# Kernel optimization log

Hardware: AMD Instinct MI355X
Metric: run time of the kernel (lower is better)

## Reference

```python
import jax, jax.numpy as jnp
import numpy as np
from jax import lax

B, N, C = 4, 1024, 384
H, G, K = 6, 2, 10
GD = C // G   # group dim = 192
HD = C // H   # head dim = 64
SCALE = HD ** -0.5
LN_EPS = 1e-5


def _sqdist(a, b):
    # a: [..., M, 3], b: [..., N, 3] -> squared euclid dist [..., M, N]
    return (jnp.sum(a * a, -1)[..., :, None]
            - 2.0 * jnp.einsum('...mc,...nc->...mn', a, b)
            + jnp.sum(b * b, -1)[..., None, :])


def _layernorm(x, g, b):
    mu = jnp.mean(x, -1, keepdims=True)
    var = jnp.mean(jnp.square(x - mu), -1, keepdims=True)
    return (x - mu) * lax.rsqrt(var + LN_EPS) * g + b


def _forward(q, q_pos, Wq, Wk, Wv, Wvoff, W1, b1, ln_g, ln_b, W2, Wproj, bproj):
    # self-attention path: v = q, v_pos = q_pos
    bidx = jnp.arange(B)[:, None, None]
    # KNN over positions: idx [B, N, K]
    d = _sqdist(q_pos, q_pos)
    _, idx = lax.top_k(-d, K)
    qp = q @ Wq                       # [B, N, C]
    v_off = q @ Wvoff                 # [B, N, C]
    local_v = v_off[bidx, idx]        # [B, N, K, C]
    # split channels into groups: 'b n k (g c) -> b g n k c'
    off_local_v = local_v.reshape(B, N, K, G, GD).transpose(0, 3, 1, 2, 4)
    group_q = qp.reshape(B, N, G, GD).transpose(0, 2, 1, 3)      # [B, G, N, GD]
    shift_feat = jnp.concatenate(
        [off_local_v, jnp.broadcast_to(group_q[:, :, :, None, :], (B, G, N, K, GD))], -1)
    h = _layernorm(shift_feat @ W1 + b1, ln_g, ln_b)
    h = jax.nn.gelu(h, approximate=False)
    offset = jnp.tanh(h @ W2)                                    # [B, G, N, K, 3]
    local_v_pos = q_pos[bidx, idx]                               # [B, N, K, 3]
    shift_pos = (local_v_pos[:, None] + offset).reshape(B, G, N * K, 3)
    # three_nn: 3 nearest v_pos points for each shifted point (squared dists, as in CUDA kernel)
    v_pos_g = jnp.broadcast_to(q_pos[:, None], (B, G, N, 3))
    d2 = _sqdist(shift_pos, v_pos_g)                             # [B, G, N*K, N]
    neg_d3, idx3 = lax.top_k(-d2, 3)
    dist3 = -neg_d3                                              # ascending
    rec = 1.0 / (dist3 + 1e-8)
    w = rec / jnp.sum(rec, -1, keepdims=True)                    # [B, G, N*K, 3]
    # three_interpolate on grouped v features
    v_g = q.reshape(B, N, G, GD).transpose(0, 2, 1, 3)           # [B, G, N, GD]
    gathered = v_g[jnp.arange(B)[:, None, None, None],
                   jnp.arange(G)[None, :, None, None], idx3]      # [B, G, N*K, 3, GD]
    interp = jnp.sum(w[..., None] * gathered, 3)                 # [B, G, N*K, GD]
    # '(b g) (n k) c -> b n k (g c)'
    interp = interp.reshape(B, G, N, K, GD).transpose(0, 2, 3, 1, 4).reshape(B, N, K, C)
    # local cross attention: 1 query vs K keys per token per head
    kk = (interp @ Wk).reshape(B, N, K, H, HD)
    vv = (interp @ Wv).reshape(B, N, K, H, HD)
    qh = qp.reshape(B, N, H, HD)
    attn = jnp.einsum('bnhd,bnkhd->bnhk', qh, kk) * SCALE
    attn = jax.nn.softmax(attn, -1)
    out = jnp.einsum('bnhk,bnkhd->bnhd', attn, vv).reshape(B, N, C)
    return out @ Wproj + bproj


def setup_inputs() -> dict:
    key = jax.random.key(0)
    ks = jax.random.split(key, 12)
    s = 0.02
    return {
        'q': jax.random.normal(ks[0], (B, N, C), jnp.float32),
        'q_pos': jax.random.normal(ks[1], (B, N, 3), jnp.float32),
        'Wq': s * jax.random.normal(ks[2], (C, C), jnp.float32),
        'Wk': s * jax.random.normal(ks[3], (C, C), jnp.float32),
        'Wv': s * jax.random.normal(ks[4], (C, C), jnp.float32),
        'Wvoff': s * jax.random.normal(ks[5], (C, C), jnp.float32),
        'W1': s * jax.random.normal(ks[6], (2 * GD, C), jnp.float32),
        'b1': jnp.zeros((C,), jnp.float32),
        'ln_g': jnp.ones((C,), jnp.float32),
        'ln_b': jnp.zeros((C,), jnp.float32),
        'W2': s * jax.random.normal(ks[7], (C, 3), jnp.float32),
        'Wproj': s * jax.random.normal(ks[8], (C, C), jnp.float32),
        'bproj': jnp.zeros((C,), jnp.float32),
    }


def reference(q, q_pos, Wq, Wk, Wv, Wvoff, W1, b1, ln_g, ln_b, W2, Wproj, bproj):
    return _forward(q, q_pos, Wq, Wk, Wv, Wvoff, W1, b1, ln_g, ln_b, W2, Wproj, bproj)
```

## Files before the change

kernel.cpp:

```cpp
#include <hip/hip_runtime.h>
#include <math.h>

constexpr int B_ = 4;
constexpr int N_ = 1024;
constexpr int C_ = 384;
constexpr int G_ = 2;
constexpr int K_ = 10;
constexpr int GD_ = 192;
constexpr int NK_ = N_ * K_;
constexpr int M2_ = B_ * G_ * N_ * K_;
constexpr float SCALE_ = 0.125f;
constexpr float MARGIN_ = 4e-4f;

__device__ __forceinline__ bool lless(double da, int ia, double db, int ib) {
  return (da < db) || (da == db && ia < ib);
}
__device__ __forceinline__ void lmin2(double& rd, int& ri, double ad, int ai,
                                      double bd, int bi) {
  bool t = lless(bd, bi, ad, ai);
  rd = t ? bd : ad; ri = t ? bi : ai;
}
__device__ __forceinline__ void lmax2(double& rd, int& ri, double ad, int ai,
                                      double bd, int bi) {
  bool t = lless(ad, ai, bd, bi);
  rd = t ? bd : ad; ri = t ? bi : ai;
}
__device__ __forceinline__ bool llessf(float da, int ia, float db, int ib) {
  return (da < db) || (da == db && ia < ib);
}
__device__ __forceinline__ void lmin2f(float& rd, int& ri, float ad, int ai,
                                       float bd, int bi) {
  bool t = llessf(bd, bi, ad, ai);
  rd = t ? bd : ad; ri = t ? bi : ai;
}
__device__ __forceinline__ void lmax2f(float& rd, int& ri, float ad, int ai,
                                       float bd, int bi) {
  bool t = llessf(ad, ai, bd, bi);
  rd = t ? bd : ad; ri = t ? bi : ai;
}

__global__ void k_zero(int* __restrict__ cnt) { cnt[0] = 0; }

__global__ void k_sqnorm2(const float* __restrict__ q_pos, double* __restrict__ s64,
                          float* __restrict__ s32) {
  int i = blockIdx.x * blockDim.x + threadIdx.x;
  if (i >= B_ * N_) return;
  double x = q_pos[3 * i], y = q_pos[3 * i + 1], z = q_pos[3 * i + 2];
  double v = x * x + y * y + z * z;
  s64[i] = v;
  s32[i] = (float)v;
}

__global__ __launch_bounds__(256) void k_knn10_w(const float* __restrict__ q_pos,
                                                 const double* __restrict__ s,
                                                 int* __restrict__ idx10) {
  int wid = (blockIdx.x * blockDim.x + threadIdx.x) >> 6;
  int lane = threadIdx.x & 63;
  if (wid >= B_ * N_) return;
  int b = wid / N_;
  double px = q_pos[3 * wid], py = q_pos[3 * wid + 1], pz = q_pos[3 * wid + 2];
  double sm = s[wid];
  const float* bp = q_pos + b * N_ * 3;
  const double* bs = s + b * N_;
  double d[K_]; int ix[K_];
  #pragma unroll
  for (int j = 0; j < K_; j++) { d[j] = INFINITY; ix[j] = 0x7fffffff; }
  for (int n0 = 0; n0 < N_; n0 += 64) {
    int n = n0 + lane;
    double dot = px * (double)bp[3 * n] + py * (double)bp[3 * n + 1] +
                 pz * (double)bp[3 * n + 2];
    double v = (sm - 2.0 * dot) + bs[n];
    bool c[K_];
    #pragma unroll
    for (int j = 0; j < K_; j++) c[j] = lless(v, n, d[j], ix[j]);
    #pragma unroll
    for (int j = K_ - 1; j >= 1; j--) {
      d[j]  = c[j] ? (c[j - 1] ? d[j - 1] : v) : d[j];
      ix[j] = c[j] ? (c[j - 1] ? ix[j - 1] : n) : ix[j];
    }
    d[0]  = c[0] ? v : d[0];
    ix[0] = c[0] ? n : ix[0];
  }
  #pragma unroll
  for (int off = 1; off < 64; off <<= 1) {
    double bd[K_]; int bi[K_];
    #pragma unroll
    for (int j = 0; j < K_; j++) {
      bd[j] = __shfl_xor(d[j], off);
      bi[j] = __shfl_xor(ix[j], off);
    }
    double md[K_]; int mi[K_];
    #pragma unroll
    for (int r = 0; r < K_; r++) {
      double m; int mj;
      lmin2(m, mj, d[r], ix[r], bd[r], bi[r]);
      #pragma unroll
      for (int j = 1; j <= r; j++) {
        double t; int ti;
        lmax2(t, ti, d[j - 1], ix[j - 1], bd[r - j], bi[r - j]);
        lmin2(m, mj, m, mj, t, ti);
      }
      md[r] = m; mi[r] = mj;
    }
    #pragma unroll
    for (int j = 0; j < K_; j++) { d[j] = md[j]; ix[j] = mi[j]; }
  }
  if (lane == 0) {
    #pragma unroll
    for (int j = 0; j < K_; j++) idx10[wid * K_ + j] = ix[j];
  }
}

template <int TM>
__global__ __launch_bounds__(384) void k_gemmSA(const float* __restrict__ A,
                                                const float* __restrict__ W,
                                                const float* __restrict__ bias,
                                                float* __restrict__ out, int M) {
  int c = threadIdx.x;
  int r0 = blockIdx.x * TM;
  float acc[TM];
  #pragma unroll
  for (int r = 0; r < TM; r++) acc[r] = 0.f;
  #pragma unroll 4
  for (int j = 0; j < C_; j++) {
    float w = W[j * C_ + c];
    #pragma unroll
    for (int r = 0; r < TM; r++) acc[r] = fmaf(A[(r0 + r) * C_ + j], w, acc[r]);
  }
  float bv = bias ? bias[c] : 0.f;
  #pragma unroll
  for (int r = 0; r < TM; r++) out[(r0 + r) * C_ + c] = acc[r] + bv;
}

__global__ __launch_bounds__(384) void k_prepM(const float* __restrict__ Wvoff,
                                               const float* __restrict__ Wq,
                                               const float* __restrict__ W1,
                                               float* __restrict__ M1f,
                                               float* __restrict__ M2f) {
  int g = blockIdx.x / C_;
  int k = blockIdx.x % C_;
  int c = threadIdx.x;
  const float* wv = Wvoff + k * C_ + g * GD_;
  const float* wq = Wq + k * C_ + g * GD_;
  double a1 = 0.0, a2 = 0.0;
  for (int d = 0; d < GD_; d++) {
    a1 += (double)wv[d] * (double)W1[d * C_ + c];
    a2 += (double)wq[d] * (double)W1[(GD_ + d) * C_ + c];
  }
  M1f[(g * C_ + k) * C_ + c] = (float)a1;
  M2f[(g * C_ + k) * C_ + c] = (float)a2;
}

template <int TM>
__global__ __launch_bounds__(384) void k_Y32(const float* __restrict__ q,
                                             const float* __restrict__ M1f,
                                             const float* __restrict__ M2f,
                                             float* __restrict__ Y1f,
                                             float* __restrict__ Y2f) {
  int c = threadIdx.x;
  int g = blockIdx.y;
  int r0 = blockIdx.x * TM;
  float a1[TM], a2[TM];
  #pragma unroll
  for (int r = 0; r < TM; r++) { a1[r] = 0.f; a2[r] = 0.f; }
  const float* m1 = M1f + (size_t)(g * C_) * C_ + c;
  const float* m2 = M2f + (size_t)(g * C_) * C_ + c;
  for (int k = 0; k < C_; k++) {
    float v1 = m1[(size_t)k * C_];
    float v2 = m2[(size_t)k * C_];
    #pragma unroll
    for (int r = 0; r < TM; r++) {
      float av = q[(r0 + r) * C_ + k];
      a1[r] = fmaf(av, v1, a1[r]);
      a2[r] = fmaf(av, v2, a2[r]);
    }
  }
  #pragma unroll
  for (int r = 0; r < TM; r++) {
    Y1f[((size_t)(r0 + r) * G_ + g) * C_ + c] = a1[r];
    Y2f[((size_t)(r0 + r) * G_ + g) * C_ + c] = a2[r];
  }
}

__global__ __launch_bounds__(256) void k_mlp32(const float* __restrict__ Y1f,
                                               const float* __restrict__ Y2f,
                                               const int* __restrict__ idx10,
                                               const float* __restrict__ q_pos,
                                               const float* __restrict__ b1,
                                               const float* __restrict__ ln_g,
                                               const float* __restrict__ ln_b,
                                               const float* __restrict__ W2,
                                               float* __restrict__ shift32) {
  int w_ = threadIdx.x >> 6, l = threadIdx.x & 63;
  int row = blockIdx.x * 4 + w_;
  int k = row % K_; int t = row / K_;
  int n = t % N_; t /= N_;
  int g = t % G_; int b = t / G_;
  int j = idx10[(b * N_ + n) * K_ + k];
  const float* y1 = Y1f + ((size_t)(b * N_ + j) * G_ + g) * C_;
  const float* y2 = Y2f + ((size_t)(b * N_ + n) * G_ + g) * C_;
  float x[6];
  #pragma unroll
  for (int jj = 0; jj < 6; jj++) {
    int col = l + 64 * jj;
    x[jj] = y1[col] + y2[col] + b1[col];
  }
  float sum = ((((x[0] + x[1]) + x[2]) + x[3]) + x[4]) + x[5];
  #pragma unroll
  for (int off = 1; off < 64; off <<= 1) sum += __shfl_xor(sum, off);
  float mu = sum * (1.0f / 384.0f);
  float sq = 0.f;
  #pragma unroll
  for (int jj = 0; jj < 6; jj++) { float dd = x[jj] - mu; sq = fmaf(dd, dd, sq); }
  #pragma unroll
  for (int off = 1; off < 64; off <<= 1) sq += __shfl_xor(sq, off);
  float var = sq * (1.0f / 384.0f);
  float rstd = 1.0f / sqrtf(var + 1e-5f);
  float ge[6];
  #pragma unroll
  for (int jj = 0; jj < 6; jj++) {
    int col = l + 64 * jj;
    float nv = (x[jj] - mu) * rstd * ln_g[col] + ln_b[col];
    ge[jj] = 0.5f * nv * (1.0f + erff(nv * 0.70710678118654752f));
  }
  float o3[3];
  #pragma unroll
  for (int o = 0; o < 3; o++) {
    float p = 0.f;
    #pragma unroll
    for (int jj = 0; jj < 6; jj++) {
      int col = l + 64 * jj;
      p = fmaf(ge[jj], W2[col * 3 + o], p);
    }
    #pragma unroll
    for (int off = 1; off < 64; off <<= 1) p += __shfl_xor(p, off);
    o3[o] = tanhf(p);
  }
  if (l == 0) {
    int gi = b * N_ + j;
    shift32[(size_t)row * 3 + 0] = q_pos[gi * 3 + 0] + o3[0];
    shift32[(size_t)row * 3 + 1] = q_pos[gi * 3 + 1] + o3[1];
    shift32[(size_t)row * 3 + 2] = q_pos[gi * 3 + 2] + o3[2];
  }
}

__global__ __launch_bounds__(256) void k_top4(const float* __restrict__ shift32,
                                              const float* __restrict__ q_pos,
                                              const float* __restrict__ s32,
                                              const float* __restrict__ q,
                                              float* __restrict__ interp,
                                              int* __restrict__ flags,
                                              int* __restrict__ cnt) {
  int wid = (blockIdx.x * blockDim.x + threadIdx.x) >> 6;
  int lane = threadIdx.x & 63;
  int m = wid % NK_; int t = wid / NK_;
  int g = t % G_; int b = t / G_;
  float px = shift32[(size_t)wid * 3], py = shift32[(size_t)wid * 3 + 1],
        pz = shift32[(size_t)wid * 3 + 2];
  float sp = px * px + py * py + pz * pz;
  const float* bp = q_pos + b * N_ * 3;
  const float* bs = s32 + b * N_;
  float d[4]; int ix[4];
  #pragma unroll
  for (int j = 0; j < 4; j++) { d[j] = INFINITY; ix[j] = 0x7fffffff; }
  for (int n0 = 0; n0 < N_; n0 += 64) {
    int n = n0 + lane;
    float dot = px * bp[3 * n] + py * bp[3 * n + 1] + pz * bp[3 * n + 2];
    float v = (sp - 2.0f * dot) + bs[n];
    bool c[4];
    #pragma unroll
    for (int j = 0; j < 4; j++) c[j] = llessf(v, n, d[j], ix[j]);
    #pragma unroll
    for (int j = 3; j >= 1; j--) {
      d[j]  = c[j] ? (c[j - 1] ? d[j - 1] : v) : d[j];
      ix[j] = c[j] ? (c[j - 1] ? ix[j - 1] : n) : ix[j];
    }
    d[0]  = c[0] ? v : d[0];
    ix[0] = c[0] ? n : ix[0];
  }
  #pragma unroll
  for (int off = 1; off < 64; off <<= 1) {
    float bd[4]; int bi[4];
    #pragma unroll
    for (int j = 0; j < 4; j++) {
      bd[j] = __shfl_xor(d[j], off);
      bi[j] = __shfl_xor(ix[j], off);
    }
    float md[4]; int mi[4];
    #pragma unroll
    for (int r = 0; r < 4; r++) {
      float mm; int mj;
      lmin2f(mm, mj, d[r], ix[r], bd[r], bi[r]);
      #pragma unroll
      for (int j = 1; j <= r; j++) {
        float tt; int ti;
        lmax2f(tt, ti, d[j - 1], ix[j - 1], bd[r - j], bi[r - j]);
        lmin2f(mm, mj, mm, mj, tt, ti);
      }
      md[r] = mm; mi[r] = mj;
    }
    #pragma unroll
    for (int j = 0; j < 4; j++) { d[j] = md[j]; ix[j] = mi[j]; }
  }
  if (d[3] - d[2] < MARGIN_) {
    if (lane == 0) {
      int pos = atomicAdd(cnt, 1);
      flags[pos] = wid;
    }
    return;
  }
  float r0 = 1.0f / (d[0] + 1e-8f);
  float r1 = 1.0f / (d[1] + 1e-8f);
  float r2 = 1.0f / (d[2] + 1e-8f);
  float rs = (r0 + r1) + r2;
  float w0 = r0 / rs, w1 = r1 / rs, w2 = r2 / rs;
  const float* qb = q + (size_t)b * N_ * C_ + g * GD_;
  const float* p0 = qb + (size_t)ix[0] * C_;
  const float* p1 = qb + (size_t)ix[1] * C_;
  const float* p2 = qb + (size_t)ix[2] * C_;
  int n_ = m / K_, k_ = m % K_;
  float* op = interp + (((size_t)(b * N_ + n_) * K_ + k_) * C_) + g * GD_;
  #pragma unroll
  for (int cc0 = 0; cc0 < GD_; cc0 += 64) {
    int cc = cc0 + lane;
    op[cc] = (w0 * p0[cc] + w1 * p1[cc]) + w2 * p2[cc];
  }
}

__global__ __launch_bounds__(256) void k_fix(const int* __restrict__ cnt,
                                             const int* __restrict__ flags,
                                             const float* __restrict__ q,
                                             const float* __restrict__ Wvoff,
                                             const float* __restrict__ Wq,
                                             const float* __restrict__ W1,
                                             const int* __restrict__ idx10,
                                             const float* __restrict__ q_pos,
                                             const double* __restrict__ s64,
                                             const float* __restrict__ b1,
                                             const float* __restrict__ ln_g,
                                             const float* __restrict__ ln_b,
                                             const float* __restrict__ W2,
                                             float* __restrict__ interp) {
  __shared__ double vbuf[4][2][GD_];
  int w_ = threadIdx.x >> 6;
  int gwid = blockIdx.x * 4 + w_;
  int lane = threadIdx.x & 63;
  int nwaves = gridDim.x * 4;
  int total = cnt[0];
  for (int i = gwid; i < total; i += nwaves) {
    int wid = __builtin_amdgcn_readfirstlane(flags[i]);
    int m = wid % NK_; int t = wid / NK_;
    int g = t % G_; int b = t / G_;
    int n_ = m / K_, k_ = m % K_;
    int j = __builtin_amdgcn_readfirstlane(idx10[(b * N_ + n_) * K_ + k_]);
    const float* qj = q + (size_t)(b * N_ + j) * C_;
    const float* qn = q + (size_t)(b * N_ + n_) * C_;
    const float* wvo = Wvoff + g * GD_;
    const float* wqg = Wq + g * GD_;
    double a0 = 0.0, a1 = 0.0, a2 = 0.0, b0 = 0.0, b1a = 0.0, b2 = 0.0;
    for (int tt = 0; tt < C_; tt++) {
      double qjt = (double)qj[tt];
      double qnt = (double)qn[tt];
      const float* r1 = wvo + (size_t)tt * C_;
      const float* r2 = wqg + (size_t)tt * C_;
      a0 += qjt * (double)r1[lane];
      a1 += qjt * (double)r1[lane + 64];
      a2 += qjt * (double)r1[lane + 128];
      b0 += qnt * (double)r2[lane];
      b1a += qnt * (double)r2[lane + 64];
      b2 += qnt * (double)r2[lane + 128];
    }
    vbuf[w_][0][lane] = a0; vbuf[w_][0][lane + 64] = a1; vbuf[w_][0][lane + 128] = a2;
    vbuf[w_][1][lane] = b0; vbuf[w_][1][lane + 64] = b1a; vbuf[w_][1][lane + 128] = b2;
    double x[6];
    #pragma unroll
    for (int jj = 0; jj < 6; jj++) x[jj] = 0.0;
    for (int d = 0; d < GD_; d++) {
      double v1d = vbuf[w_][0][d];
      double v2d = vbuf[w_][1][d];
      const float* w1t = W1 + (size_t)d * C_;
      const float* w1b = W1 + (size_t)(GD_ + d) * C_;
      #pragma unroll
      for (int jj = 0; jj < 6; jj++) {
        int col = lane + 64 * jj;
        x[jj] += v1d * (double)w1t[col] + v2d * (double)w1b[col];
      }
    }
    #pragma unroll
    for (int jj = 0; jj < 6; jj++) x[jj] += (double)b1[lane + 64 * jj];
    double sum = ((((x[0] + x[1]) + x[2]) + x[3]) + x[4]) + x[5];
    #pragma unroll
    for (int off = 1; off < 64; off <<= 1) sum += __shfl_xor(sum, off);
    double mu = sum / 384.0;
    double sq = 0.0;
    #pragma unroll
    for (int jj = 0; jj < 6; jj++) { double dd = x[jj] - mu; sq += dd * dd; }
    #pragma unroll
    for (int off = 1; off < 64; off <<= 1) sq += __shfl_xor(sq, off);
    double var = sq / 384.0;
    double rstd = 1.0 / sqrt(var + 1e-5);
    double ge[6];
    #pragma unroll
    for (int jj = 0; jj < 6; jj++) {
      int col = lane + 64 * jj;
      double nv = (x[jj] - mu) * rstd * (double)ln_g[col] + (double)ln_b[col];
      ge[jj] = 0.5 * nv * (1.0 + erf(nv * 0.70710678118654752440));
    }
    double o3[3];
    #pragma unroll
    for (int o = 0; o < 3; o++) {
      double p = 0.0;
      #pragma unroll
      for (int jj = 0; jj < 6; jj++) {
        int col = lane + 64 * jj;
        p += ge[jj] * (double)W2[col * 3 + o];
      }
      #pragma unroll
      for (int off = 1; off < 64; off <<= 1) p += __shfl_xor(p, off);
      o3[o] = tanh(p);
    }
    int gi = b * N_ + j;
    double px = (double)q_pos[gi * 3 + 0] + o3[0];
    double py = (double)q_pos[gi * 3 + 1] + o3[1];
    double pz = (double)q_pos[gi * 3 + 2] + o3[2];
    double sp = px * px + py * py + pz * pz;
    const float* bp = q_pos + b * N_ * 3;
    const double* bs = s64 + b * N_;
    double d0 = INFINITY, d1 = INFINITY, d2 = INFINITY;
    int i0 = 0x7fffffff, i1 = 0x7fffffff, i2 = 0x7fffffff;
    for (int n = lane; n < N_; n += 64) {
      double dot = px * (double)bp[3 * n] + py * (double)bp[3 * n + 1] +
                   pz * (double)bp[3 * n + 2];
      double dd = (sp - 2.0 * dot) + bs[n];
      bool c0 = lless(dd, n, d0, i0);
      bool c1 = lless(dd, n, d1, i1);
      bool c2 = lless(dd, n, d2, i2);
      double nd2 = c2 ? (c1 ? d1 : dd) : d2; int ni2 = c2 ? (c1 ? i1 : n) : i2;
      double nd1 = c1 ? (c0 ? d0 : dd) : d1; int ni1 = c1 ? (c0 ? i0 : n) : i1;
      double nd0 = c0 ? dd : d0;             int ni0 = c0 ? n : i0;
      d0 = nd0; d1 = nd1; d2 = nd2; i0 = ni0; i1 = ni1; i2 = ni2;
    }
    #pragma unroll
    for (int off = 1; off < 64; off <<= 1) {
      double e0 = __shfl_xor(d0, off), e1 = __shfl_xor(d1, off), e2 = __shfl_xor(d2, off);
      int j0 = __shfl_xor(i0, off), j1 = __shfl_xor(i1, off), j2 = __shfl_xor(i2, off);
      double mnd, mxd, p1d, q1d, q2d, q3d, q4d, t1d, t2d;
      int mni, mxi, p1i, q1i, q2i, q3i, q4i, t1i, t2i;
      lmin2(mnd, mni, d0, i0, e0, j0);
      lmax2(mxd, mxi, d0, i0, e0, j0);
      lmin2(p1d, p1i, d1, i1, e1, j1);
      lmin2(t1d, t1i, p1d, p1i, mxd, mxi);
      lmax2(q1d, q1i, d1, i1, e0, j0);
      lmax2(q2d, q2i, d0, i0, e1, j1);
      lmin2(q3d, q3i, q1d, q1i, q2d, q2i);
      lmin2(q4d, q4i, d2, i2, e2, j2);
      lmin2(t2d, t2i, q3d, q3i, q4d, q4i);
      d0 = mnd; i0 = mni; d1 = t1d; i1 = t1i; d2 = t2d; i2 = t2i;
    }
    double r0 = 1.0 / (d0 + 1e-8);
    double r1 = 1.0 / (d1 + 1e-8);
    double r2 = 1.0 / (d2 + 1e-8);
    double rs = (r0 + r1) + r2;
    float w0 = (float)(r0 / rs), w1 = (float)(r1 / rs), w2 = (float)(r2 / rs);
    const float* qb = q + (size_t)b * N_ * C_ + g * GD_;
    const float* p0 = qb + (size_t)i0 * C_;
    const float* p1 = qb + (size_t)i1 * C_;
    const float* p2 = qb + (size_t)i2 * C_;
    float* op = interp + (((size_t)(b * N_ + n_) * K_ + k_) * C_) + g * GD_;
    #pragma unroll
    for (int cc0 = 0; cc0 < GD_; cc0 += 64) {
      int cc = cc0 + lane;
      op[cc] = (w0 * p0[cc] + w1 * p1[cc]) + w2 * p2[cc];
    }
  }
}

__global__ __launch_bounds__(256) void k_T(const float* __restrict__ Wk,
                                           float* __restrict__ WkT) {
  int i = blockIdx.x * blockDim.x + threadIdx.x;
  if (i >= C_ * C_) return;
  int r = i / C_, c = i % C_;
  WkT[c * C_ + r] = Wk[i];
}

template <int TM>
__global__ __launch_bounds__(384) void k_U(const float* __restrict__ qp,
                                           const float* __restrict__ WkT,
                                           float* __restrict__ U) {
  int c = threadIdx.x;
  int r0 = blockIdx.x * TM;
  for (int h = 0; h < 6; h++) {
    float acc[TM];
    #pragma unroll
    for (int r = 0; r < TM; r++) acc[r] = 0.f;
    #pragma unroll 4
    for (int dd = 0; dd < 64; dd++) {
      float w = WkT[(h * 64 + dd) * C_ + c];
      #pragma unroll
      for (int r = 0; r < TM; r++)
        acc[r] = fmaf(qp[(r0 + r) * C_ + h * 64 + dd], w, acc[r]);
    }
    #pragma unroll
    for (int r = 0; r < TM; r++) U[((size_t)(r0 + r) * 6 + h) * C_ + c] = acc[r];
  }
}

__global__ __launch_bounds__(256) void k_attn2(const float* __restrict__ interp,
                                               float* __restrict__ Umix) {
  int wid = blockIdx.x * 4 + (threadIdx.x >> 6);
  int lane = threadIdx.x & 63;
  int bn = wid / 6;
  float* urow = Umix + (size_t)wid * C_;
  float u[6];
  #pragma unroll
  for (int j = 0; j < 6; j++) u[j] = urow[lane + 64 * j];
  float logit[K_];
  #pragma unroll
  for (int k = 0; k < K_; k++) {
    const float* ip = interp + ((size_t)bn * K_ + k) * C_;
    float p = 0.f;
    #pragma unroll
    for (int j = 0; j < 6; j++) p = fmaf(ip[lane + 64 * j], u[j], p);
    #pragma unroll
    for (int off = 1; off < 64; off <<= 1) p += __shfl_xor(p, off);
    logit[k] = p * SCALE_;
  }
  float mx = logit[0];
  #pragma unroll
  for (int k = 1; k < K_; k++) mx = fmaxf(mx, logit[k]);
  float e[K_], se = 0.f;
  #pragma unroll
  for (int k = 0; k < K_; k++) { e[k] = expf(logit[k] - mx); se += e[k]; }
  float inv = 1.0f / se;
  #pragma unroll
  for (int k = 0; k < K_; k++) e[k] *= inv;
  #pragma unroll
  for (int j = 0; j < 6; j++) {
    float mv = 0.f;
    #pragma unroll
    for (int k = 0; k < K_; k++)
      mv = fmaf(e[k], interp[((size_t)bn * K_ + k) * C_ + lane + 64 * j], mv);
    urow[lane + 64 * j] = mv;
  }
}

template <int TM>
__global__ __launch_bounds__(384) void k_out(const float* __restrict__ mix,
                                             const float* __restrict__ Wv,
                                             float* __restrict__ attn_out) {
  int c = threadIdx.x;
  int h = __builtin_amdgcn_readfirstlane(threadIdx.x) >> 6;
  int r0 = blockIdx.x * TM;
  float acc[TM];
  #pragma unroll
  for (int r = 0; r < TM; r++) acc[r] = 0.f;
  #pragma unroll 4
  for (int ci = 0; ci < C_; ci++) {
    float w = Wv[ci * C_ + c];
    #pragma unroll
    for (int r = 0; r < TM; r++)
      acc[r] = fmaf(mix[((size_t)(r0 + r) * 6 + h) * C_ + ci], w, acc[r]);
  }
  #pragma unroll
  for (int r = 0; r < TM; r++) attn_out[(size_t)(r0 + r) * C_ + c] = acc[r];
}

extern "C" void kernel_launch(void* const* d_in, const int* in_sizes, int n_in,
                              void* d_out, int out_size, void* d_ws, size_t ws_size,
                              hipStream_t stream) {
  const float* q     = (const float*)d_in[0];
  const float* q_pos = (const float*)d_in[1];
  const float* Wq    = (const float*)d_in[2];
  const float* Wk    = (const float*)d_in[3];
  const float* Wv    = (const float*)d_in[4];
  const float* Wvoff = (const float*)d_in[5];
  const float* W1    = (const float*)d_in[6];
  const float* b1    = (const float*)d_in[7];
  const float* ln_g  = (const float*)d_in[8];
  const float* ln_b  = (const float*)d_in[9];
  const float* W2    = (const float*)d_in[10];
  const float* Wproj = (const float*)d_in[11];
  const float* bproj = (const float*)d_in[12];
  float* out = (float*)d_out;

  char* ws = (char*)d_ws;
  char* U0 = ws; ws += 38 * 1024 * 1024;
  float* Y1f     = (float*)(U0);
  float* Y2f     = (float*)(U0 + 12582912);
  float* M1f     = (float*)(U0 + 25165824);
  float* M2f     = (float*)(U0 + 26345472);
  float* shift32 = (float*)(U0 + 27525120);
  int*   idx10   = (int*)  (U0 + 28508160);
  int*   flags   = (int*)  (U0 + 28672000);
  float* s32     = (float*)(U0 + 28999680);
  int*   cnt     = (int*)  (U0 + 29016064);
  float* Umix    = (float*)U0;
  double* s64    = (double*)ws; ws += (size_t)B_ * N_ * 8;
  float*  qp32   = (float*)ws;  ws += (size_t)B_ * N_ * C_ * 4;
  float*  interp = (float*)ws;  ws += (size_t)B_ * N_ * K_ * C_ * 4;
  float*  WkT    = (float*)ws;  ws += (size_t)C_ * C_ * 4;
  float*  attn_out = qp32;

  k_zero<<<1, 1, 0, stream>>>(cnt);
  k_sqnorm2<<<(B_ * N_ + 255) / 256, 256, 0, stream>>>(q_pos, s64, s32);
  k_knn10_w<<<B_ * N_ / 4, 256, 0, stream>>>(q_pos, s64, idx10);
  k_gemmSA<8><<<B_ * N_ / 8, 384, 0, stream>>>(q, Wq, nullptr, qp32, B_ * N_);
  k_prepM<<<G_ * C_, 384, 0, stream>>>(Wvoff, Wq, W1, M1f, M2f);
  k_Y32<8><<<dim3(B_ * N_ / 8, G_), 384, 0, stream>>>(q, M1f, M2f, Y1f, Y2f);
  k_mlp32<<<M2_ / 4, 256, 0, stream>>>(Y1f, Y2f, idx10, q_pos, b1, ln_g, ln_b, W2,
                                       shift32);
  k_top4<<<M2_ / 4, 256, 0, stream>>>(shift32, q_pos, s32, q, interp, flags, cnt);
  k_fix<<<512, 256, 0, stream>>>(cnt, flags, q, Wvoff, Wq, W1, idx10, q_pos, s64,
                                 b1, ln_g, ln_b, W2, interp);
  k_T<<<(C_ * C_ + 255) / 256, 256, 0, stream>>>(Wk, WkT);
  k_U<8><<<B_ * N_ / 8, 384, 0, stream>>>(qp32, WkT, Umix);
  k_attn2<<<B_ * N_ * 6 / 4, 256, 0, stream>>>(interp, Umix);
  k_out<8><<<B_ * N_ / 8, 384, 0, stream>>>(Umix, Wv, attn_out);
  k_gemmSA<8><<<B_ * N_ / 8, 384, 0, stream>>>(attn_out, Wproj, bproj, out, B_ * N_);
}
```

Baseline: 738.9 us.

## Fuse offset MLP with three-NN search and pack positions as float4

Merges the offset-MLP kernel and the top-4 nearest-neighbour kernel into one, so each wave uses its shifted point straight from registers and the shift32 buffer round trip plus one launch go away. Positions and squared norms are packed into a float4 array, so each candidate costs one vector load, and the distance is computed with FMAs using a prescaled -2p. The lexicographic index tie-break in the insertion and merge steps becomes a plain float comparison, which makes the comparisons cheaper but can choose differently when distances tie exactly. Ties near the cutoff are still sent to the fix-up path through the margin check.

```diff
diff --git a/kernel.cpp b/kernel.cpp
--- a/kernel.cpp
+++ b/kernel.cpp
@@ -25,30 +25,27 @@
   bool t = lless(ad, ai, bd, bi);
   rd = t ? bd : ad; ri = t ? bi : ai;
 }
-__device__ __forceinline__ bool llessf(float da, int ia, float db, int ib) {
-  return (da < db) || (da == db && ia < ib);
-}
-__device__ __forceinline__ void lmin2f(float& rd, int& ri, float ad, int ai,
-                                       float bd, int bi) {
-  bool t = llessf(bd, bi, ad, ai);
+__device__ __forceinline__ void pmin2(float& rd, int& ri, float ad, int ai,
+                                      float bd, int bi) {
+  bool t = bd < ad;
   rd = t ? bd : ad; ri = t ? bi : ai;
 }
-__device__ __forceinline__ void lmax2f(float& rd, int& ri, float ad, int ai,
-                                       float bd, int bi) {
-  bool t = llessf(ad, ai, bd, bi);
+__device__ __forceinline__ void pmax2(float& rd, int& ri, float ad, int ai,
+                                      float bd, int bi) {
+  bool t = ad < bd;
   rd = t ? bd : ad; ri = t ? bi : ai;
 }
 
 __global__ void k_zero(int* __restrict__ cnt) { cnt[0] = 0; }
 
-__global__ void k_sqnorm2(const float* __restrict__ q_pos, double* __restrict__ s64,
-                          float* __restrict__ s32) {
+__global__ void k_prep0(const float* __restrict__ q_pos, double* __restrict__ s64,
+                        float4* __restrict__ pos4) {
   int i = blockIdx.x * blockDim.x + threadIdx.x;
   if (i >= B_ * N_) return;
-  double x = q_pos[3 * i], y = q_pos[3 * i + 1], z = q_pos[3 * i + 2];
-  double v = x * x + y * y + z * z;
+  float x = q_pos[3 * i], y = q_pos[3 * i + 1], z = q_pos[3 * i + 2];
+  double v = (double)x * x + (double)y * y + (double)z * z;
   s64[i] = v;
-  s32[i] = (float)v;
+  pos4[i] = make_float4(x, y, z, (float)v);
 }
 
 __global__ __launch_bounds__(256) void k_knn10_w(const float* __restrict__ q_pos,
@@ -182,15 +179,19 @@
   }
 }
 
-__global__ __launch_bounds__(256) void k_mlp32(const float* __restrict__ Y1f,
-                                               const float* __restrict__ Y2f,
-                                               const int* __restrict__ idx10,
-                                               const float* __restrict__ q_pos,
-                                               const float* __restrict__ b1,
-                                               const float* __restrict__ ln_g,
-                                               const float* __restrict__ ln_b,
-                                               const float* __restrict__ W2,
-                                               float* __restrict__ shift32) {
+__global__ __launch_bounds__(256) void k_mlptop4(const float* __restrict__ Y1f,
+                                                 const float* __restrict__ Y2f,
+                                                 const int* __restrict__ idx10,
+                                                 const float* __restrict__ q_pos,
+                                                 const float* __restrict__ b1,
+                                                 const float* __restrict__ ln_g,
+                                                 const float* __restrict__ ln_b,
+                                                 const float* __restrict__ W2,
+                                                 const float4* __restrict__ pos4,
+                                                 const float* __restrict__ q,
+                                                 float* __restrict__ interp,
+                                                 int* __restrict__ flags,
+                                                 int* __restrict__ cnt) {
   int w_ = threadIdx.x >> 6, l = threadIdx.x & 63;
   int row = blockIdx.x * 4 + w_;
   int k = row % K_; int t = row / K_;
@@ -236,76 +237,58 @@
     for (int off = 1; off < 64; off <<= 1) p += __shfl_xor(p, off);
     o3[o] = tanhf(p);
   }
-  if (l == 0) {
-    int gi = b * N_ + j;
-    shift32[(size_t)row * 3 + 0] = q_pos[gi * 3 + 0] + o3[0];
-    shift32[(size_t)row * 3 + 1] = q_pos[gi * 3 + 1] + o3[1];
-    shift32[(size_t)row * 3 + 2] = q_pos[gi * 3 + 2] + o3[2];
-  }
-}
-
-__global__ __launch_bounds__(256) void k_top4(const float* __restrict__ shift32,
-                                              const float* __restrict__ q_pos,
-                                              const float* __restrict__ s32,
-                                              const float* __restrict__ q,
-                                              float* __restrict__ interp,
-                                              int* __restrict__ flags,
-                                              int* __restrict__ cnt) {
-  int wid = (blockIdx.x * blockDim.x + threadIdx.x) >> 6;
-  int lane = threadIdx.x & 63;
-  int m = wid % NK_; int t = wid / NK_;
-  int g = t % G_; int b = t / G_;
-  float px = shift32[(size_t)wid * 3], py = shift32[(size_t)wid * 3 + 1],
-        pz = shift32[(size_t)wid * 3 + 2];
-  float sp = px * px + py * py + pz * pz;
-  const float* bp = q_pos + b * N_ * 3;
-  const float* bs = s32 + b * N_;
+  int gi = b * N_ + j;
+  float px = q_pos[gi * 3 + 0] + o3[0];
+  float py = q_pos[gi * 3 + 1] + o3[1];
+  float pz = q_pos[gi * 3 + 2] + o3[2];
+  float sp = fmaf(px, px, fmaf(py, py, pz * pz));
+  float nx = -2.0f * px, ny = -2.0f * py, nz = -2.0f * pz;
+  const float4* p4 = pos4 + b * N_;
   float d[4]; int ix[4];
   #pragma unroll
-  for (int j = 0; j < 4; j++) { d[j] = INFINITY; ix[j] = 0x7fffffff; }
+  for (int jj = 0; jj < 4; jj++) { d[jj] = INFINITY; ix[jj] = 0x7fffffff; }
   for (int n0 = 0; n0 < N_; n0 += 64) {
-    int n = n0 + lane;
-    float dot = px * bp[3 * n] + py * bp[3 * n + 1] + pz * bp[3 * n + 2];
-    float v = (sp - 2.0f * dot) + bs[n];
-    bool c[4];
-    #pragma unroll
-    for (int j = 0; j < 4; j++) c[j] = llessf(v, n, d[j], ix[j]);
-    #pragma unroll
-    for (int j = 3; j >= 1; j--) {
-      d[j]  = c[j] ? (c[j - 1] ? d[j - 1] : v) : d[j];
-      ix[j] = c[j] ? (c[j - 1] ? ix[j - 1] : n) : ix[j];
-    }
-    d[0]  = c[0] ? v : d[0];
-    ix[0] = c[0] ? n : ix[0];
+    int nn = n0 + l;
+    float4 pv = p4[nn];
+    float v = fmaf(nx, pv.x, fmaf(ny, pv.y, fmaf(nz, pv.z, sp + pv.w)));
+    bool c0 = v < d[0], c1 = v < d[1], c2 = v < d[2], c3 = v < d[3];
+    d[3]  = c3 ? (c2 ? d[2] : v) : d[3];
+    ix[3] = c3 ? (c2 ? ix[2] : nn) : ix[3];
+    d[2]  = c2 ? (c1 ? d[1] : v) : d[2];
+    ix[2] = c2 ? (c1 ? ix[1] : nn) : ix[2];
+    d[1]  = c1 ? (c0 ? d[0] : v) : d[1];
+    ix[1] = c1 ? (c0 ? ix[0] : nn) : ix[1];
+    d[0]  = c0 ? v : d[0];
+    ix[0] = c0 ? nn : ix[0];
   }
   #pragma unroll
   for (int off = 1; off < 64; off <<= 1) {
     float bd[4]; int bi[4];
     #pragma unroll
-    for (int j = 0; j < 4; j++) {
-      bd[j] = __shfl_xor(d[j], off);
-      bi[j] = __shfl_xor(ix[j], off);
+    for (int jj = 0; jj < 4; jj++) {
+      bd[jj] = __shfl_xor(d[jj], off);
+      bi[jj] = __shfl_xor(ix[jj], off);
     }
     float md[4]; int mi[4];
     #pragma unroll
     for (int r = 0; r < 4; r++) {
       float mm; int mj;
-      lmin2f(mm, mj, d[r], ix[r], bd[r], bi[r]);
+      pmin2(mm, mj, d[r], ix[r], bd[r], bi[r]);
       #pragma unroll
-      for (int j = 1; j <= r; j++) {
+      for (int jj = 1; jj <= r; jj++) {
         float tt; int ti;
-        lmax2f(tt, ti, d[j - 1], ix[j - 1], bd[r - j], bi[r - j]);
-        lmin2f(mm, mj, mm, mj, tt, ti);
+        pmax2(tt, ti, d[jj - 1], ix[jj - 1], bd[r - jj], bi[r - jj]);
+        pmin2(mm, mj, mm, mj, tt, ti);
       }
       md[r] = mm; mi[r] = mj;
     }
     #pragma unroll
-    for (int j = 0; j < 4; j++) { d[j] = md[j]; ix[j] = mi[j]; }
+    for (int jj = 0; jj < 4; jj++) { d[jj] = md[jj]; ix[jj] = mi[jj]; }
   }
   if (d[3] - d[2] < MARGIN_) {
-    if (lane == 0) {
+    if (l == 0) {
       int pos = atomicAdd(cnt, 1);
-      flags[pos] = wid;
+      flags[pos] = row;
     }
     return;
   }
@@ -318,11 +301,10 @@
   const float* p0 = qb + (size_t)ix[0] * C_;
   const float* p1 = qb + (size_t)ix[1] * C_;
   const float* p2 = qb + (size_t)ix[2] * C_;
-  int n_ = m / K_, k_ = m % K_;
-  float* op = interp + (((size_t)(b * N_ + n_) * K_ + k_) * C_) + g * GD_;
+  float* op = interp + (((size_t)(b * N_ + n) * K_ + k) * C_) + g * GD_;
   #pragma unroll
   for (int cc0 = 0; cc0 < GD_; cc0 += 64) {
-    int cc = cc0 + lane;
+    int cc = cc0 + l;
     op[cc] = (w0 * p0[cc] + w1 * p1[cc]) + w2 * p2[cc];
   }
 }
@@ -585,16 +567,15 @@
 
   char* ws = (char*)d_ws;
   char* U0 = ws; ws += 38 * 1024 * 1024;
-  float* Y1f     = (float*)(U0);
-  float* Y2f     = (float*)(U0 + 12582912);
-  float* M1f     = (float*)(U0 + 25165824);
-  float* M2f     = (float*)(U0 + 26345472);
-  float* shift32 = (float*)(U0 + 27525120);
-  int*   idx10   = (int*)  (U0 + 28508160);
-  int*   flags   = (int*)  (U0 + 28672000);
-  float* s32     = (float*)(U0 + 28999680);
-  int*   cnt     = (int*)  (U0 + 29016064);
-  float* Umix    = (float*)U0;
+  float*  Y1f    = (float*)(U0);
+  float*  Y2f    = (float*)(U0 + 12582912);
+  float*  M1f    = (float*)(U0 + 25165824);
+  float*  M2f    = (float*)(U0 + 26345472);
+  int*    idx10  = (int*)  (U0 + 28508160);
+  int*    flags  = (int*)  (U0 + 28672000);
+  float4* pos4   = (float4*)(U0 + 28999680);
+  int*    cnt    = (int*)  (U0 + 29065216);
+  float*  Umix   = (float*)U0;
   double* s64    = (double*)ws; ws += (size_t)B_ * N_ * 8;
   float*  qp32   = (float*)ws;  ws += (size_t)B_ * N_ * C_ * 4;
   float*  interp = (float*)ws;  ws += (size_t)B_ * N_ * K_ * C_ * 4;
@@ -602,14 +583,13 @@
   float*  attn_out = qp32;
 
   k_zero<<<1, 1, 0, stream>>>(cnt);
-  k_sqnorm2<<<(B_ * N_ + 255) / 256, 256, 0, stream>>>(q_pos, s64, s32);
+  k_prep0<<<(B_ * N_ + 255) / 256, 256, 0, stream>>>(q_pos, s64, pos4);
   k_knn10_w<<<B_ * N_ / 4, 256, 0, stream>>>(q_pos, s64, idx10);
   k_gemmSA<8><<<B_ * N_ / 8, 384, 0, stream>>>(q, Wq, nullptr, qp32, B_ * N_);
   k_prepM<<<G_ * C_, 384, 0, stream>>>(Wvoff, Wq, W1, M1f, M2f);
   k_Y32<8><<<dim3(B_ * N_ / 8, G_), 384, 0, stream>>>(q, M1f, M2f, Y1f, Y2f);
-  k_mlp32<<<M2_ / 4, 256, 0, stream>>>(Y1f, Y2f, idx10, q_pos, b1, ln_g, ln_b, W2,
-                                       shift32);
-  k_top4<<<M2_ / 4, 256, 0, stream>>>(shift32, q_pos, s32, q, interp, flags, cnt);
+  k_mlptop4<<<M2_ / 4, 256, 0, stream>>>(Y1f, Y2f, idx10, q_pos, b1, ln_g, ln_b,
+                                         W2, pos4, q, interp, flags, cnt);
   k_fix<<<512, 256, 0, stream>>>(cnt, flags, q, Wvoff, Wq, W1, idx10, q_pos, s64,
                                  b1, ln_g, ln_b, W2, interp);
   k_T<<<(C_ * C_ + 255) / 256, 256, 0, stream>>>(Wk, WkT);
```

New measurement: 660.1 us. -10.7%, faster.
